# Kernel optimization log

Measured on AMD Instinct MI355X. Metric: run time of the kernel, lower is better.

The kernel has to match this reference:

```python
import jax, jax.numpy as jnp
import numpy as np

B, N, D_IN, D_HID, D_OUT = 8, 512, 4608, 4608, 1152
DROP = 0.1
INV_SQRT2 = 0.7071067811865476
INV_SQRT_2PI = 0.3989422804014327


def _clean(s):
    # nan -> 1e-5, inf -> 1.0 (matches torch.where chain)
    return jnp.where(jnp.isnan(s), jnp.asarray(1e-5, s.dtype),
                     jnp.where(jnp.isinf(s), jnp.asarray(1.0, s.dtype), s))


def kl_regularizer(w_mu, w_sigma):
    d = w_mu.shape[0]
    ws = jax.nn.softplus(w_sigma)  # log(1+exp(w_sigma))
    return 0.5 * jnp.mean(d * ws + jnp.sum(w_mu * w_mu, axis=0) - d - d * jnp.log(ws))


def vdp_linear(mu_in, Sigma_in, w_mu, w_sigma):
    mu_out = jnp.matmul(mu_in, w_mu)                                 # [B,N,U]
    kl = kl_regularizer(w_mu, w_sigma)
    W_Sigma = jax.nn.softplus(w_sigma)                               # [U]
    Sigma_1 = jnp.matmul(Sigma_in, w_mu * w_mu)                      # w^T Sigma_in w (diag)
    Sigma_2 = jnp.sum(mu_in * mu_in, axis=-1, keepdims=True) * W_Sigma
    Sigma_3 = jnp.sum(Sigma_in, axis=-1, keepdims=True) * W_Sigma
    return mu_out, _clean(Sigma_1 + Sigma_2 + Sigma_3), kl


def vdp_gelu(mu_in, Sigma_in):
    # exact (erf) gelu and its analytic derivative: Phi(x) + x*phi(x)
    cdf = 0.5 * (1.0 + jax.lax.erf(mu_in * INV_SQRT2))
    pdf = jnp.exp(-0.5 * mu_in * mu_in) * INV_SQRT_2PI
    grad = cdf + mu_in * pdf
    return mu_in * cdf, grad * grad * Sigma_in


def vdp_dropout(mu_in, Sigma_in, mask):
    keep = 1.0 - DROP
    m = mask.astype(mu_in.dtype)
    mu_out = mu_in * m / keep                       # torch F.dropout scaling
    Sigma_out = Sigma_in * m / mu_in.shape[-1]      # kept Sigma values (unscaled), / units
    return mu_out, _clean(Sigma_out)


def setup_inputs() -> dict:
    key = jax.random.key(0)
    k = jax.random.split(key, 8)
    mu_in = jax.random.normal(k[0], (B, N, D_IN), dtype=jnp.float32)
    sigma_in = jax.random.uniform(k[1], (B, N, D_IN), dtype=jnp.float32)
    mask1 = jax.random.bernoulli(k[2], 1.0 - DROP, (B, N, D_HID))
    mask2 = jax.random.bernoulli(k[3], 1.0 - DROP, (B, N, D_OUT))
    w_mu1 = 0.05 * jax.random.normal(k[4], (D_IN, D_HID), dtype=jnp.float32)
    w_sigma1 = jnp.full((D_HID,), -4.6, dtype=jnp.float32)
    w_mu2 = 0.05 * jax.random.normal(k[5], (D_HID, D_OUT), dtype=jnp.float32)
    w_sigma2 = jnp.full((D_OUT,), -4.6, dtype=jnp.float32)
    return {"mu_in": mu_in, "sigma_in": sigma_in, "mask1": mask1, "mask2": mask2,
            "w_mu1": w_mu1, "w_sigma1": w_sigma1, "w_mu2": w_mu2, "w_sigma2": w_sigma2}


def reference(mu_in, sigma_in, mask1, mask2, w_mu1, w_sigma1, w_mu2, w_sigma2):
    mu, sig, kl1 = vdp_linear(mu_in, sigma_in, w_mu1, w_sigma1)
    mu, sig = vdp_gelu(mu, sig)
    mu, sig = vdp_dropout(mu, sig, mask1)
    mu, sig, kl2 = vdp_linear(mu, sig, w_mu2, w_sigma2)
    mu, sig = vdp_dropout(mu, sig, mask2)
    return mu, _clean(sig), kl1 + kl2
```

## Files before the change

kernel.cpp:

```cpp
#include <hip/hip_runtime.h>
#include <cstdint>
#include <cstddef>

static constexpr int Mrows = 4096;
static constexpr int K1 = 4608;
static constexpr int N1 = 4608;
static constexpr int N2 = 1152;
static constexpr int NPART1 = (K1 / 64) * (N1 / 64);
static constexpr int NPART2 = (K1 / 64) * (N2 / 64);

typedef float  f32x4  __attribute__((ext_vector_type(4)));
typedef __bf16 bf16x8 __attribute__((ext_vector_type(8)));
typedef unsigned short u16x8 __attribute__((ext_vector_type(8)));

__device__ __forceinline__ unsigned short f2bf(float f) {
  unsigned int u = __float_as_uint(f);
  u += 0x7fffu + ((u >> 16) & 1u);
  return (unsigned short)(u >> 16);
}
__device__ __forceinline__ float bf2f(unsigned short h) {
  return __uint_as_float(((unsigned int)h) << 16);
}
__device__ __forceinline__ float cleanf(float s) {
  if (__builtin_isnan(s)) return 1e-5f;
  if (__builtin_isinf(s)) return 1.0f;
  return s;
}

__global__ __launch_bounds__(256) void prep_in(
    const float* __restrict__ mu, const float* __restrict__ sg,
    unsigned short* __restrict__ A1, unsigned short* __restrict__ As16,
    float* __restrict__ rmu2, float* __restrict__ rsg)
{
  const int row = blockIdx.x;
  const int tid = threadIdx.x;
  const float4* mup = (const float4*)(mu + (size_t)row * K1);
  const float4* sgp = (const float4*)(sg + (size_t)row * K1);
  ushort4* a1p = (ushort4*)(A1 + (size_t)row * K1);
  ushort4* asp = (ushort4*)(As16 + (size_t)row * K1);
  float smu = 0.f, ssg = 0.f;
  for (int j = tid; j < K1 / 4; j += 256) {
    float4 m4 = mup[j];
    float4 s4 = sgp[j];
    smu += m4.x*m4.x + m4.y*m4.y + m4.z*m4.z + m4.w*m4.w;
    ssg += s4.x + s4.y + s4.z + s4.w;
    a1p[j] = make_ushort4(f2bf(m4.x), f2bf(m4.y), f2bf(m4.z), f2bf(m4.w));
    asp[j] = make_ushort4(f2bf(s4.x), f2bf(s4.y), f2bf(s4.z), f2bf(s4.w));
  }
  __shared__ float red[2][4];
  for (int off = 32; off; off >>= 1) {
    smu += __shfl_down(smu, off);
    ssg += __shfl_down(ssg, off);
  }
  const int lane = tid & 63, wv = tid >> 6;
  if (!lane) { red[0][wv] = smu; red[1][wv] = ssg; }
  __syncthreads();
  if (tid == 0) {
    rmu2[row] = red[0][0] + red[0][1] + red[0][2] + red[0][3];
    rsg[row]  = red[1][0] + red[1][1] + red[1][2] + red[1][3];
  }
}

__global__ __launch_bounds__(256) void prep_w2x(
    const float* __restrict__ w1, const float* __restrict__ w2,
    unsigned short* __restrict__ B1t, unsigned short* __restrict__ B1sq,
    unsigned short* __restrict__ B2t, unsigned short* __restrict__ B2sq,
    float* __restrict__ part1, float* __restrict__ part2)
{
  const int ybl = blockIdx.y;
  const bool is2 = ybl >= (N1 / 64);
  const int nb = is2 ? (ybl - N1 / 64) : ybl;
  const float* w = is2 ? w2 : w1;
  unsigned short* Bt = is2 ? B2t : B1t;
  unsigned short* Bq = is2 ? B2sq : B1sq;
  float* parts = is2 ? part2 : part1;
  const int N = is2 ? N2 : N1;

  const int kt = blockIdx.x * 64;
  const int nt = nb * 64;
  const int tid = threadIdx.x;

  __shared__ float t[64][65];
  float loc = 0.f;
  {
    const int r = tid >> 4;
    const int c = (tid & 15) * 4;
#pragma unroll
    for (int p = 0; p < 4; ++p) {
      const int k = p * 16 + r;
      float4 v = *(const float4*)(w + (size_t)(kt + k) * N + nt + c);
      t[k][c] = v.x; t[k][c + 1] = v.y; t[k][c + 2] = v.z; t[k][c + 3] = v.w;
      loc += v.x*v.x + v.y*v.y + v.z*v.z + v.w*v.w;
    }
  }
  __syncthreads();
  {
    const int kk = (tid & 7) * 8;
#pragma unroll
    for (int q = 0; q < 2; ++q) {
      const int n = (tid >> 3) + q * 32;
      u16x8 bt, bq;
#pragma unroll
      for (int i = 0; i < 8; ++i) {
        float v = t[kk + i][n];
        bt[i] = f2bf(v);
        bq[i] = f2bf(v * v);
      }
      size_t o = (size_t)(nt + n) * K1 + (kt + kk);
      *(u16x8*)(Bt + o) = bt;
      *(u16x8*)(Bq + o) = bq;
    }
  }
  __shared__ float red[4];
  for (int off = 32; off; off >>= 1) loc += __shfl_down(loc, off);
  const int lane = tid & 63, wv = tid >> 6;
  if (!lane) red[wv] = loc;
  __syncthreads();
  if (tid == 0)
    parts[nb * (K1 / 64) + blockIdx.x] = red[0] + red[1] + red[2] + red[3];
}

__global__ __launch_bounds__(256) void kl_prep(
    const float* __restrict__ wsig1, const float* __restrict__ wsig2,
    const float* __restrict__ part1, const float* __restrict__ part2,
    float* __restrict__ ws1, float* __restrict__ ws2, float* __restrict__ outkl)
{
  const int tid = threadIdx.x;
  float s1 = 0.f, l1 = 0.f, s2 = 0.f, l2 = 0.f, q1 = 0.f, q2 = 0.f;
  for (int j = tid; j < N1; j += 256) {
    float x = wsig1[j];
    float sp = (x > 20.f) ? x : log1pf(expf(x));
    ws1[j] = sp; s1 += sp; l1 += logf(sp);
  }
  for (int j = tid; j < N2; j += 256) {
    float x = wsig2[j];
    float sp = (x > 20.f) ? x : log1pf(expf(x));
    ws2[j] = sp; s2 += sp; l2 += logf(sp);
  }
  for (int j = tid; j < NPART1; j += 256) q1 += part1[j];
  for (int j = tid; j < NPART2; j += 256) q2 += part2[j];
  __shared__ float red[6][4];
  for (int off = 32; off; off >>= 1) {
    s1 += __shfl_down(s1, off); l1 += __shfl_down(l1, off);
    s2 += __shfl_down(s2, off); l2 += __shfl_down(l2, off);
    q1 += __shfl_down(q1, off); q2 += __shfl_down(q2, off);
  }
  const int lane = tid & 63, wv = tid >> 6;
  if (!lane) {
    red[0][wv] = s1; red[1][wv] = l1; red[2][wv] = s2;
    red[3][wv] = l2; red[4][wv] = q1; red[5][wv] = q2;
  }
  __syncthreads();
  if (tid == 0) {
    float S1v = red[0][0] + red[0][1] + red[0][2] + red[0][3];
    float L1v = red[1][0] + red[1][1] + red[1][2] + red[1][3];
    float S2v = red[2][0] + red[2][1] + red[2][2] + red[2][3];
    float L2v = red[3][0] + red[3][1] + red[3][2] + red[3][3];
    float Q1v = red[4][0] + red[4][1] + red[4][2] + red[4][3];
    float Q2v = red[5][0] + red[5][1] + red[5][2] + red[5][3];
    const float d = 4608.f;
    float kl1 = 0.5f * (d * (S1v / (float)N1) + Q1v / (float)N1 - d - d * (L1v / (float)N1));
    float kl2 = 0.5f * (d * (S2v / (float)N2) + Q2v / (float)N2 - d - d * (L2v / (float)N2));
    outkl[0] = kl1 + kl2;
  }
}

#define GLD16(gp, lp) __builtin_amdgcn_global_load_lds( \
    (__attribute__((address_space(1))) void*)(unsigned short*)(gp), \
    (__attribute__((address_space(3))) void*)(lp), 16, 0, 0)

__device__ __forceinline__ void storeC(float v, float* p) { *p = v; }
__device__ __forceinline__ void storeC(float v, unsigned short* p) { *p = f2bf(v); }

template <int NT, typename CT, bool FUSE>
__global__ __launch_bounds__(512, 2) void gemm256(
    const unsigned short* __restrict__ Amu, const unsigned short* __restrict__ Asg,
    const unsigned short* __restrict__ Bmu, const unsigned short* __restrict__ Bsq,
    CT* __restrict__ Cmu, CT* __restrict__ Csg,
    const int* __restrict__ mask2, const float* __restrict__ ws2,
    const float* __restrict__ r2mu, const float* __restrict__ r2sg)
{
  __shared__ __align__(16) char smem[114688];
  char* lA = smem;
  char* lB = smem + 65536;

  const int tid  = threadIdx.x;
  const int lane = tid & 63;
  const int wave = tid >> 6;
  const int which = blockIdx.z;
  const unsigned short* Ag = which ? Asg : Amu;
  const unsigned short* Bg = which ? Bsq : Bmu;
  CT* Cg = which ? Csg : Cmu;

  const int m0 = blockIdx.y * 256;
  const int n0 = blockIdx.x * 192;
  const int wm = (wave >> 2) * 128;
  const int wn = (wave & 3) * 48;
  const int fm = lane & 15;
  const int kq = lane >> 4;

  const int rbase = tid >> 3;
  const int gg = (tid & 7) ^ (rbase & 7);
  const unsigned short* gA0 = Ag + (size_t)(m0 + rbase) * K1 + gg * 8;
  const unsigned short* gB0 = Bg + (size_t)(n0 + rbase) * K1 + gg * 8;

  auto stA = [&](int buf, int h, int kt2) {
    const unsigned short* g = gA0 + (size_t)h * 128 * K1 + (size_t)kt2 * 64;
    char* l = lA + buf * 32768 + h * 16384 + tid * 16;
    GLD16(g, l);
    GLD16(g + (size_t)64 * K1, l + 8192);
  };
  auto stB = [&](int buf, int kt2) {
    const unsigned short* g = gB0 + (size_t)kt2 * 64;
    char* l = lB + buf * 24576 + tid * 16;
    GLD16(g, l);
    GLD16(g + (size_t)64 * K1, l + 8192);
    GLD16(g + (size_t)128 * K1, l + 16384);
  };

  const int abase = (wm + fm) * 128;
  const int bbase = 65536 + (wn + fm) * 128;
  const int x0 = ((0 * 4 + kq) ^ (fm & 7)) * 16;
  const int x1 = ((1 * 4 + kq) ^ (fm & 7)) * 16;

  f32x4 acc[8][3];
#pragma unroll
  for (int i = 0; i < 8; ++i)
#pragma unroll
    for (int j = 0; j < 3; ++j) acc[i][j] = (f32x4){0.f, 0.f, 0.f, 0.f};

  stB(0, 0);
  stA(0, 0, 0); stA(0, 1, 0);
  stB(1, 1);
  asm volatile("s_waitcnt vmcnt(3)" ::: "memory");
  __builtin_amdgcn_s_barrier();

  const int ksteps = K1 / 64;
  for (int kt = 0; kt < ksteps; ++kt) {
    const int cur = kt & 1;
    const char* cA = lA + cur * 32768 + abase;
    const char* cB = smem + cur * 24576 + bbase;

    bf16x8 Af[8][2], Bf[3][2];

#pragma unroll
    for (int j = 0; j < 3; ++j) {
      Bf[j][0] = *(const bf16x8*)(cB + j * 2048 + x0);
      Bf[j][1] = *(const bf16x8*)(cB + j * 2048 + x1);
    }
#pragma unroll
    for (int i = 0; i < 4; ++i) {
      Af[i][0] = *(const bf16x8*)(cA + i * 2048 + x0);
      Af[i][1] = *(const bf16x8*)(cA + i * 2048 + x1);
    }
    if (kt + 1 < ksteps) stA(cur ^ 1, 0, kt + 1);
    asm volatile("s_waitcnt lgkmcnt(8)" ::: "memory");
    __builtin_amdgcn_s_barrier();
    asm volatile("s_waitcnt lgkmcnt(0)" ::: "memory");
    __builtin_amdgcn_s_setprio(1);
#pragma unroll
    for (int i = 0; i < 4; ++i)
#pragma unroll
      for (int j = 0; j < 2; ++j) {
        acc[i][j] = __builtin_amdgcn_mfma_f32_16x16x32_bf16(Af[i][0], Bf[j][0], acc[i][j], 0, 0, 0);
        acc[i][j] = __builtin_amdgcn_mfma_f32_16x16x32_bf16(Af[i][1], Bf[j][1], acc[i][j], 0, 0, 0);
      }
    __builtin_amdgcn_s_setprio(0);
    __builtin_amdgcn_s_barrier();

#pragma unroll
    for (int i = 4; i < 8; ++i) {
      Af[i][0] = *(const bf16x8*)(cA + i * 2048 + x0);
      Af[i][1] = *(const bf16x8*)(cA + i * 2048 + x1);
    }
    if (kt + 1 < ksteps) stA(cur ^ 1, 1, kt + 1);
    __builtin_amdgcn_s_barrier();
    asm volatile("s_waitcnt lgkmcnt(0)" ::: "memory");
    __builtin_amdgcn_s_setprio(1);
#pragma unroll
    for (int i = 4; i < 8; ++i)
#pragma unroll
      for (int j = 0; j < 2; ++j) {
        acc[i][j] = __builtin_amdgcn_mfma_f32_16x16x32_bf16(Af[i][0], Bf[j][0], acc[i][j], 0, 0, 0);
        acc[i][j] = __builtin_amdgcn_mfma_f32_16x16x32_bf16(Af[i][1], Bf[j][1], acc[i][j], 0, 0, 0);
      }
    __builtin_amdgcn_s_setprio(0);
    __builtin_amdgcn_s_barrier();

    if (kt + 2 < ksteps) stB(cur, kt + 2);
    __builtin_amdgcn_s_barrier();
    __builtin_amdgcn_s_setprio(1);
#pragma unroll
    for (int i = 0; i < 8; ++i) {
      acc[i][2] = __builtin_amdgcn_mfma_f32_16x16x32_bf16(Af[i][0], Bf[2][0], acc[i][2], 0, 0, 0);
      acc[i][2] = __builtin_amdgcn_mfma_f32_16x16x32_bf16(Af[i][1], Bf[2][1], acc[i][2], 0, 0, 0);
    }
    __builtin_amdgcn_s_setprio(0);
    if (kt < ksteps - 2) asm volatile("s_waitcnt vmcnt(3)" ::: "memory");
    else                 asm volatile("s_waitcnt vmcnt(0)" ::: "memory");
    __builtin_amdgcn_s_barrier();
  }

  const int rr = (lane >> 4) * 4;
  const int cc = lane & 15;
  if constexpr (!FUSE) {
#pragma unroll
    for (int i = 0; i < 8; ++i) {
      const int grow = m0 + wm + i * 16 + rr;
#pragma unroll
      for (int j = 0; j < 3; ++j) {
        const int gcol = n0 + wn + j * 16 + cc;
        CT* cp = Cg + (size_t)grow * NT + gcol;
#pragma unroll
        for (int r = 0; r < 4; ++r) storeC(acc[i][j][r], cp + (size_t)r * NT);
      }
    }
  } else {
    const float inv_keep  = 1.f / 0.9f;
    const float inv_units = 1.f / 1152.f;
    float wcol[3];
    if (which) {
#pragma unroll
      for (int j = 0; j < 3; ++j) wcol[j] = ws2[n0 + wn + j * 16 + cc];
    }
#pragma unroll
    for (int i = 0; i < 8; ++i) {
#pragma unroll
      for (int r = 0; r < 4; ++r) {
        const int grow = m0 + wm + i * 16 + rr + r;
        const float rterm = which ? (r2mu[grow] + r2sg[grow]) : 0.f;
#pragma unroll
        for (int j = 0; j < 3; ++j) {
          const int gcol = n0 + wn + j * 16 + cc;
          const float mm = (float)mask2[(size_t)grow * NT + gcol];
          const float v = acc[i][j][r];
          float o;
          if (which == 0) {
            o = v * mm * inv_keep;
          } else {
            float sig4 = cleanf(v + rterm * wcol[j]);
            o = cleanf(cleanf(sig4 * mm * inv_units));
          }
          Cg[(size_t)grow * NT + gcol] = (CT)o;
        }
      }
    }
  }
}

__global__ __launch_bounds__(256) void mid_kernel(
    const unsigned short* __restrict__ mu1, const unsigned short* __restrict__ S1,
    const int* __restrict__ mask1, const float* __restrict__ ws1,
    const float* __restrict__ rmu2, const float* __restrict__ rsg,
    unsigned short* __restrict__ A2, unsigned short* __restrict__ As2,
    float* __restrict__ r2mu, float* __restrict__ r2sg)
{
  const int row = blockIdx.x;
  const int tid = threadIdx.x;
  const float rterm = rmu2[row] + rsg[row];
  const ushort4* mup = (const ushort4*)(mu1 + (size_t)row * N1);
  const ushort4* s1p = (const ushort4*)(S1 + (size_t)row * N1);
  const int4* mkp = (const int4*)(mask1 + (size_t)row * N1);
  const float4* wsp = (const float4*)ws1;
  ushort4* a2p = (ushort4*)(A2 + (size_t)row * N1);
  ushort4* as2p = (ushort4*)(As2 + (size_t)row * N1);
  float smu = 0.f, ssg = 0.f;
  for (int j = tid; j < N1 / 4; j += 256) {
    ushort4 m4 = mup[j]; ushort4 s4 = s1p[j]; int4 k4 = mkp[j]; float4 w4 = wsp[j];
    float xv[4] = {bf2f(m4.x), bf2f(m4.y), bf2f(m4.z), bf2f(m4.w)};
    float Sv[4] = {bf2f(s4.x), bf2f(s4.y), bf2f(s4.z), bf2f(s4.w)};
    float wv[4] = {w4.x, w4.y, w4.z, w4.w};
    int   kv[4] = {k4.x, k4.y, k4.z, k4.w};
    unsigned short oa[4], os[4];
#pragma unroll
    for (int t = 0; t < 4; t++) {
      float sig1 = cleanf(Sv[t] + rterm * wv[t]);
      float x = xv[t];
      float cdf = 0.5f * (1.f + erff(x * 0.70710678118654752f));
      float pdf = expf(-0.5f * x * x) * 0.3989422804014327f;
      float g = cdf + x * pdf;
      float mu2v = x * cdf;
      float sig2 = g * g * sig1;
      float mm = (float)kv[t];
      float mu3 = mu2v * mm * (1.f / 0.9f);
      float sig3 = cleanf(sig2 * mm * (1.f / 4608.f));
      smu += mu3 * mu3;
      ssg += sig3;
      oa[t] = f2bf(mu3);
      os[t] = f2bf(sig3);
    }
    a2p[j] = make_ushort4(oa[0], oa[1], oa[2], oa[3]);
    as2p[j] = make_ushort4(os[0], os[1], os[2], os[3]);
  }
  __shared__ float red[2][4];
  for (int off = 32; off; off >>= 1) {
    smu += __shfl_down(smu, off);
    ssg += __shfl_down(ssg, off);
  }
  const int lane = tid & 63, wv2 = tid >> 6;
  if (!lane) { red[0][wv2] = smu; red[1][wv2] = ssg; }
  __syncthreads();
  if (tid == 0) {
    r2mu[row] = red[0][0] + red[0][1] + red[0][2] + red[0][3];
    r2sg[row] = red[1][0] + red[1][1] + red[1][2] + red[1][3];
  }
}

extern "C" void kernel_launch(void* const* d_in, const int* in_sizes, int n_in,
                              void* d_out, int out_size, void* d_ws, size_t ws_size,
                              hipStream_t stream)
{
  const float* mu_in = (const float*)d_in[0];
  const float* sg_in = (const float*)d_in[1];
  const int* mask1 = (const int*)d_in[2];
  const int* mask2 = (const int*)d_in[3];
  const float* w_mu1 = (const float*)d_in[4];
  const float* wsig1 = (const float*)d_in[5];
  const float* w_mu2 = (const float*)d_in[6];
  const float* wsig2 = (const float*)d_in[7];
  float* out = (float*)d_out;

  char* ws = (char*)d_ws;
  const size_t oA1  = 0;
  const size_t oAs  = oA1  + (size_t)37748736;
  const size_t oB1t = oAs  + (size_t)37748736;
  const size_t oB1q = oB1t + (size_t)42467328;
  const size_t oB2t = oB1q + (size_t)42467328;
  const size_t oB2q = oB2t + (size_t)10616832;
  const size_t oMu1 = oB2q + (size_t)10616832;
  const size_t oS1  = oMu1 + (size_t)37748736;
  const size_t oVec = oS1  + (size_t)37748736;

  unsigned short* A1     = (unsigned short*)(ws + oA1);
  unsigned short* As16   = (unsigned short*)(ws + oAs);
  unsigned short* B1t    = (unsigned short*)(ws + oB1t);
  unsigned short* B1sq16 = (unsigned short*)(ws + oB1q);
  unsigned short* B2t    = (unsigned short*)(ws + oB2t);
  unsigned short* B2sq16 = (unsigned short*)(ws + oB2q);
  unsigned short* mu1b   = (unsigned short*)(ws + oMu1);
  unsigned short* S1b16  = (unsigned short*)(ws + oS1);

  float* rmu2 = (float*)(ws + oVec);
  float* rsg  = rmu2 + Mrows;
  float* r2mu = rsg + Mrows;
  float* r2sg = r2mu + Mrows;
  float* ws1v = r2sg + Mrows;
  float* ws2v = ws1v + N1;
  float* part1 = ws2v + N2;
  float* part2 = part1 + NPART1;

  prep_in<<<Mrows, 256, 0, stream>>>(mu_in, sg_in, A1, As16, rmu2, rsg);
  prep_w2x<<<dim3(K1 / 64, N1 / 64 + N2 / 64), 256, 0, stream>>>(
      w_mu1, w_mu2, B1t, B1sq16, B2t, B2sq16, part1, part2);
  kl_prep<<<1, 256, 0, stream>>>(wsig1, wsig2, part1, part2, ws1v, ws2v,
                                 out + (size_t)2 * Mrows * N2);

  gemm256<N1, unsigned short, false><<<dim3(N1 / 192, Mrows / 256, 2), 512, 0, stream>>>(
      A1, As16, B1t, B1sq16, mu1b, S1b16, nullptr, nullptr, nullptr, nullptr);

  mid_kernel<<<Mrows, 256, 0, stream>>>(mu1b, S1b16, mask1, ws1v, rmu2, rsg,
                                        A1, As16, r2mu, r2sg);

  gemm256<N2, float, true><<<dim3(N2 / 192, Mrows / 256, 2), 512, 0, stream>>>(
      A1, As16, B2t, B2sq16, out, out + (size_t)Mrows * N2,
      mask2, ws2v, r2mu, r2sg);

  (void)in_sizes; (void)n_in; (void)out_size; (void)ws_size;
}
```

Before: 826.3 us.

## Collapse three-phase GEMM k-loop into one LDS-read phase and one MFMA block

The main GEMM k-loop used to split each k-step into three phases, each with its own barriers and interleaved A-tile staging. It now reads all A and B fragments from LDS up front and issues both A-half prefetches. After a single wait and barrier it issues the next B prefetch and then runs all 48 MFMAs in one prioritized block. The goal is fewer workgroup barriers per k-step and a longer uninterrupted MFMA stream. The cost is less overlap between LDS reads and matrix math, plus bursty issue of the global-to-LDS copies.

```diff
diff --git a/kernel.cpp b/kernel.cpp
--- a/kernel.cpp
+++ b/kernel.cpp
@@ -249,53 +249,28 @@
       Bf[j][1] = *(const bf16x8*)(cB + j * 2048 + x1);
     }
 #pragma unroll
-    for (int i = 0; i < 4; ++i) {
+    for (int i = 0; i < 8; ++i) {
       Af[i][0] = *(const bf16x8*)(cA + i * 2048 + x0);
       Af[i][1] = *(const bf16x8*)(cA + i * 2048 + x1);
     }
-    if (kt + 1 < ksteps) stA(cur ^ 1, 0, kt + 1);
-    asm volatile("s_waitcnt lgkmcnt(8)" ::: "memory");
+    if (kt + 1 < ksteps) { stA(cur ^ 1, 0, kt + 1); stA(cur ^ 1, 1, kt + 1); }
+
+    asm volatile("s_waitcnt lgkmcnt(0)" ::: "memory");
+    __builtin_amdgcn_sched_barrier(0);
     __builtin_amdgcn_s_barrier();
-    asm volatile("s_waitcnt lgkmcnt(0)" ::: "memory");
+
+    if (kt + 2 < ksteps) stB(cur, kt + 2);
+
     __builtin_amdgcn_s_setprio(1);
 #pragma unroll
-    for (int i = 0; i < 4; ++i)
-#pragma unroll
-      for (int j = 0; j < 2; ++j) {
+    for (int i = 0; i < 8; ++i)
+#pragma unroll
+      for (int j = 0; j < 3; ++j) {
         acc[i][j] = __builtin_amdgcn_mfma_f32_16x16x32_bf16(Af[i][0], Bf[j][0], acc[i][j], 0, 0, 0);
         acc[i][j] = __builtin_amdgcn_mfma_f32_16x16x32_bf16(Af[i][1], Bf[j][1], acc[i][j], 0, 0, 0);
       }
     __builtin_amdgcn_s_setprio(0);
-    __builtin_amdgcn_s_barrier();
-
-#pragma unroll
-    for (int i = 4; i < 8; ++i) {
-      Af[i][0] = *(const bf16x8*)(cA + i * 2048 + x0);
-      Af[i][1] = *(const bf16x8*)(cA + i * 2048 + x1);
-    }
-    if (kt + 1 < ksteps) stA(cur ^ 1, 1, kt + 1);
-    __builtin_amdgcn_s_barrier();
-    asm volatile("s_waitcnt lgkmcnt(0)" ::: "memory");
-    __builtin_amdgcn_s_setprio(1);
-#pragma unroll
-    for (int i = 4; i < 8; ++i)
-#pragma unroll
-      for (int j = 0; j < 2; ++j) {
-        acc[i][j] = __builtin_amdgcn_mfma_f32_16x16x32_bf16(Af[i][0], Bf[j][0], acc[i][j], 0, 0, 0);
-        acc[i][j] = __builtin_amdgcn_mfma_f32_16x16x32_bf16(Af[i][1], Bf[j][1], acc[i][j], 0, 0, 0);
-      }
-    __builtin_amdgcn_s_setprio(0);
-    __builtin_amdgcn_s_barrier();
-
-    if (kt + 2 < ksteps) stB(cur, kt + 2);
-    __builtin_amdgcn_s_barrier();
-    __builtin_amdgcn_s_setprio(1);
-#pragma unroll
-    for (int i = 0; i < 8; ++i) {
-      acc[i][2] = __builtin_amdgcn_mfma_f32_16x16x32_bf16(Af[i][0], Bf[2][0], acc[i][2], 0, 0, 0);
-      acc[i][2] = __builtin_amdgcn_mfma_f32_16x16x32_bf16(Af[i][1], Bf[2][1], acc[i][2], 0, 0, 0);
-    }
-    __builtin_amdgcn_s_setprio(0);
+
     if (kt < ksteps - 2) asm volatile("s_waitcnt vmcnt(3)" ::: "memory");
     else                 asm volatile("s_waitcnt vmcnt(0)" ::: "memory");
     __builtin_amdgcn_s_barrier();
```

Measured after the change: 835.4 us. About the same (+1.1%).
